# Kernel tuning notes

Hardware: AMD Instinct MI355X
Metric: run time of the kernel (lower is better)

Reference implementation:

```python
import jax, jax.numpy as jnp
import numpy as np

T, B, I, H = 1024, 64, 3, 2048


def setup_inputs() -> dict:
    key = jax.random.key(0)
    ks = jax.random.split(key, 6)
    lim = 1.0 / np.sqrt(H).astype(np.float32)  # eqx GRUCell init range
    return {
        "inp": jax.random.normal(ks[0], (T, B, I), jnp.float32),
        "init_hidden": jax.random.normal(ks[1], (B, H), jnp.float32),
        "weight_ih": jax.random.uniform(ks[2], (3 * H, I), jnp.float32, -lim, lim),
        "weight_hh": jax.random.uniform(ks[3], (3 * H, H), jnp.float32, -lim, lim),
        "bias": jax.random.uniform(ks[4], (3 * H,), jnp.float32, -lim, lim),
        "bias_n": jax.random.uniform(ks[5], (H,), jnp.float32, -lim, lim),
    }


def reference(inp, init_hidden, weight_ih, weight_hh, bias, bias_n):
    # Input projections for all timesteps at once: [T, B, 3H]
    igates_all = jnp.einsum("tbi,gi->tbg", inp, weight_ih) + bias

    def step(h, ig):
        hg = h @ weight_hh.T  # [B, 3H]
        ig_r, ig_z, ig_n = jnp.split(ig, 3, axis=-1)
        hg_r, hg_z, hg_n = jnp.split(hg, 3, axis=-1)
        reset = jax.nn.sigmoid(ig_r + hg_r)
        upd = jax.nn.sigmoid(ig_z + hg_z)
        new = jnp.tanh(ig_n + reset * (hg_n + bias_n))
        h_new = new + upd * (h - new)  # eqx GRUCell: new + inp_gate*(hidden-new)
        return h_new, h_new[:, 0]      # out = first hidden unit per step

    _, out = jax.lax.scan(step, init_hidden, igates_all)
    return out  # [T, B]
```

## Files before the change

kernel.cpp:

```cpp
#include <hip/hip_runtime.h>

typedef __attribute__((ext_vector_type(8))) short bf16x8;
typedef __attribute__((ext_vector_type(4))) float f32x4;
typedef __attribute__((ext_vector_type(4))) int i32x4;

#define Tn 1024
#define Bn 64
#define Hn 2048
#define NBLK 256
#define NTHR 512

#define GRP(ring, leaf, g) (((((ring) << 7) | ((leaf) << 3) | (g))) * 32)

#define SPIN_LIMIT (1u << 25)

__device__ __forceinline__ unsigned short f2b(float x) {
    unsigned u = __float_as_uint(x);
    return (unsigned short)((u + 0x7fffu + ((u >> 16) & 1u)) >> 16);
}
__device__ __forceinline__ float sigm(float x) {
    return __builtin_amdgcn_rcpf(1.0f + __expf(-x));
}
__device__ __forceinline__ float tanh_f(float x) {
    float e = __expf(2.0f * x);
    return 1.0f - 2.0f * __builtin_amdgcn_rcpf(1.0f + e);
}

__device__ __forceinline__ void store_short_wt(unsigned short* p, unsigned v) {
    asm volatile("global_store_short %0, %1, off sc0 sc1" :: "v"(p), "v"(v) : "memory");
}
__device__ __forceinline__ void store_dword_wt(float* p, float v) {
    asm volatile("global_store_dword %0, %1, off sc0 sc1" :: "v"(p), "v"(__float_as_uint(v)) : "memory");
}
__device__ __forceinline__ void store_u64_wt(unsigned long long* p, unsigned long long v) {
    asm volatile("global_store_dwordx2 %0, %1, off sc0 sc1" :: "v"(p), "v"(v) : "memory");
}
__device__ __forceinline__ unsigned poll_read(unsigned* p) {
    unsigned old;
    asm volatile("global_atomic_add %0, %1, %2, off sc0 sc1\n\ts_waitcnt vmcnt(0)"
                 : "=v"(old) : "v"(p), "v"(0u) : "memory");
    return old;
}

__device__ __forceinline__ long hfrag_off(int b, int k) {
    return ((long)(((k >> 5) * 4 + (b >> 4)) * 64) + ((k >> 3) & 3) * 16 + (b & 15)) * 8 + (k & 7);
}

__global__ void prep_kernel(const float* __restrict__ init_h,
                            unsigned short* __restrict__ h0,
                            unsigned* __restrict__ ctrl) {
    const int i = blockIdx.x * 256 + threadIdx.x;
    const int b  = i >> 9;
    const int k4 = (i & 511) << 2;
    float4 v = *reinterpret_cast<const float4*>(init_h + (long)b * Hn + k4);
    unsigned long long q = (unsigned long long)f2b(v.x)
                         | ((unsigned long long)f2b(v.y) << 16)
                         | ((unsigned long long)f2b(v.z) << 32)
                         | ((unsigned long long)f2b(v.w) << 48);
    store_u64_wt((unsigned long long*)(h0 + hfrag_off(b, k4)), q);
    if (i < 8192)
        asm volatile("global_store_dword %0, %1, off sc0 sc1"
                     :: "v"(ctrl + i), "v"(0u) : "memory");
}

__global__ void __launch_bounds__(NTHR, 2) gru_kernel(
    const float* __restrict__ inp,
    const float* __restrict__ init_h,
    const float* __restrict__ w_ih,
    const float* __restrict__ w_hh,
    const float* __restrict__ bias,
    const float* __restrict__ bias_n,
    unsigned short* __restrict__ h0,
    unsigned short* __restrict__ h1,
    unsigned* __restrict__ ctrl,
    float* __restrict__ out)
{
    __shared__ f32x4 red[8][2][3][64];

    const int tid  = threadIdx.x;
    const int lane = tid & 63;
    const int w    = tid >> 6;
    const int quad = lane >> 4;
    const int n16  = lane & 15;
    const int R    = blockIdx.x & 1;
    const int c    = blockIdx.x >> 1;
    const int jg   = c * 16 + n16;
    const int ks   = w * 256;
    const int bbase = 32 * R;

    bf16x8 Bf[3][8];
    #pragma unroll
    for (int nt = 0; nt < 3; ++nt) {
        const long row = (long)(nt * Hn + jg);
        #pragma unroll
        for (int k = 0; k < 8; ++k) {
            const float* p = w_hh + row * Hn + ks + k * 32 + quad * 8;
            bf16x8 b;
            #pragma unroll
            for (int j = 0; j < 8; ++j) b[j] = (short)f2b(p[j]);
            Bf[nt][k] = b;
        }
    }

    float wr0 = w_ih[jg*3+0], wr1 = w_ih[jg*3+1], wr2 = w_ih[jg*3+2];
    float wz0 = w_ih[(Hn+jg)*3+0], wz1 = w_ih[(Hn+jg)*3+1], wz2 = w_ih[(Hn+jg)*3+2];
    float wn0 = w_ih[(2*Hn+jg)*3+0], wn1 = w_ih[(2*Hn+jg)*3+1], wn2 = w_ih[(2*Hn+jg)*3+2];
    float br_ = bias[jg], bz_ = bias[Hn+jg], bn2_ = bias[2*Hn+jg];
    float bnn_ = bias_n[jg];

    float hst[4];
    if (w < 2) {
        #pragma unroll
        for (int r = 0; r < 4; ++r)
            hst[r] = init_h[(long)(bbase + 16 * w + quad * 4 + r) * Hn + jg];
    }

    const int kkE = c >> 1;
    const int qE  = (c & 1) * 2 + (n16 >> 3);
    const int eE  = n16 & 7;

    const int leafC = c >> 3;
    const int grp   = c >> 4;

    for (int t = 0; t < Tn; ++t) {
        const unsigned short* hcur = (t & 1) ? h1 : h0;
        unsigned short* hnext      = (t & 1) ? h0 : h1;

        float xv[4][3];
        if (w < 2) {
            #pragma unroll
            for (int r = 0; r < 4; ++r) {
                const float* xp = inp + ((long)t * Bn + bbase + 16 * w + quad * 4 + r) * 3;
                xv[r][0] = xp[0]; xv[r][1] = xp[1]; xv[r][2] = xp[2];
            }
        }

        f32x4 acc[2][3];
        #pragma unroll
        for (int m = 0; m < 2; ++m)
            #pragma unroll
            for (int nt = 0; nt < 3; ++nt)
                acc[m][nt] = f32x4{0.f, 0.f, 0.f, 0.f};

        if (lane == 0 && t) {
            const unsigned tgt = (unsigned)(t << 4);
            unsigned spins = 0;
            while (poll_read(&ctrl[GRP(R, leafC, w)]) < tgt) {
                __builtin_amdgcn_s_sleep(1);
                if (++spins > SPIN_LIMIT) break;
            }
        }

        const unsigned short* pa = hcur + ((long)(32 * w + 2 * R) * 64 + lane) * 8;

        i32x4 hb[16];
        #pragma unroll
        for (int kki = 0; kki < 8; ++kki) {
            #pragma unroll
            for (int m = 0; m < 2; ++m) {
                asm volatile("global_load_dwordx4 %0, %1, off sc0 sc1"
                             : "=v"(hb[kki * 2 + m])
                             : "v"(pa + (long)(kki * 4 + m) * 512) : "memory");
            }
        }
        asm volatile("s_waitcnt vmcnt(12)"
                     : "+v"(hb[0]), "+v"(hb[1]), "+v"(hb[2]), "+v"(hb[3])
                     :: "memory");
        __builtin_amdgcn_s_setprio(1);
        #pragma unroll
        for (int kki = 0; kki < 2; ++kki) {
            #pragma unroll
            for (int m = 0; m < 2; ++m) {
                union { i32x4 q; bf16x8 v; } u;
                u.q = hb[kki * 2 + m];
                bf16x8 a = u.v;
                acc[m][0] = __builtin_amdgcn_mfma_f32_16x16x32_bf16(a, Bf[0][kki], acc[m][0], 0, 0, 0);
                acc[m][1] = __builtin_amdgcn_mfma_f32_16x16x32_bf16(a, Bf[1][kki], acc[m][1], 0, 0, 0);
                acc[m][2] = __builtin_amdgcn_mfma_f32_16x16x32_bf16(a, Bf[2][kki], acc[m][2], 0, 0, 0);
            }
        }
        __builtin_amdgcn_s_setprio(0);
        asm volatile("s_waitcnt vmcnt(8)"
                     : "+v"(hb[4]), "+v"(hb[5]), "+v"(hb[6]), "+v"(hb[7])
                     :: "memory");
        __builtin_amdgcn_s_setprio(1);
        #pragma unroll
        for (int kki = 2; kki < 4; ++kki) {
            #pragma unroll
            for (int m = 0; m < 2; ++m) {
                union { i32x4 q; bf16x8 v; } u;
                u.q = hb[kki * 2 + m];
                bf16x8 a = u.v;
                acc[m][0] = __builtin_amdgcn_mfma_f32_16x16x32_bf16(a, Bf[0][kki], acc[m][0], 0, 0, 0);
                acc[m][1] = __builtin_amdgcn_mfma_f32_16x16x32_bf16(a, Bf[1][kki], acc[m][1], 0, 0, 0);
                acc[m][2] = __builtin_amdgcn_mfma_f32_16x16x32_bf16(a, Bf[2][kki], acc[m][2], 0, 0, 0);
            }
        }
        __builtin_amdgcn_s_setprio(0);
        asm volatile("s_waitcnt vmcnt(4)"
                     : "+v"(hb[8]), "+v"(hb[9]), "+v"(hb[10]), "+v"(hb[11])
                     :: "memory");
        __builtin_amdgcn_s_setprio(1);
        #pragma unroll
        for (int kki = 4; kki < 6; ++kki) {
            #pragma unroll
            for (int m = 0; m < 2; ++m) {
                union { i32x4 q; bf16x8 v; } u;
                u.q = hb[kki * 2 + m];
                bf16x8 a = u.v;
                acc[m][0] = __builtin_amdgcn_mfma_f32_16x16x32_bf16(a, Bf[0][kki], acc[m][0], 0, 0, 0);
                acc[m][1] = __builtin_amdgcn_mfma_f32_16x16x32_bf16(a, Bf[1][kki], acc[m][1], 0, 0, 0);
                acc[m][2] = __builtin_amdgcn_mfma_f32_16x16x32_bf16(a, Bf[2][kki], acc[m][2], 0, 0, 0);
            }
        }
        __builtin_amdgcn_s_setprio(0);
        asm volatile("s_waitcnt vmcnt(0)"
                     : "+v"(hb[12]), "+v"(hb[13]), "+v"(hb[14]), "+v"(hb[15])
                     :: "memory");
        __builtin_amdgcn_s_setprio(1);
        #pragma unroll
        for (int kki = 6; kki < 8; ++kki) {
            #pragma unroll
            for (int m = 0; m < 2; ++m) {
                union { i32x4 q; bf16x8 v; } u;
                u.q = hb[kki * 2 + m];
                bf16x8 a = u.v;
                acc[m][0] = __builtin_amdgcn_mfma_f32_16x16x32_bf16(a, Bf[0][kki], acc[m][0], 0, 0, 0);
                acc[m][1] = __builtin_amdgcn_mfma_f32_16x16x32_bf16(a, Bf[1][kki], acc[m][1], 0, 0, 0);
                acc[m][2] = __builtin_amdgcn_mfma_f32_16x16x32_bf16(a, Bf[2][kki], acc[m][2], 0, 0, 0);
            }
        }
        __builtin_amdgcn_s_setprio(0);

        #pragma unroll
        for (int m = 0; m < 2; ++m)
            #pragma unroll
            for (int nt = 0; nt < 3; ++nt)
                red[w][m][nt][lane] = acc[m][nt];
        __syncthreads();

        if (w < 2) {
            f32x4 s0 = red[0][w][0][lane], s1 = red[0][w][1][lane], s2 = red[0][w][2][lane];
            #pragma unroll
            for (int src = 1; src < 8; ++src) {
                s0 += red[src][w][0][lane];
                s1 += red[src][w][1][lane];
                s2 += red[src][w][2][lane];
            }
            #pragma unroll
            for (int r = 0; r < 4; ++r) {
                const int b = bbase + 16 * w + quad * 4 + r;
                float pr = br_ + wr0*xv[r][0] + wr1*xv[r][1] + wr2*xv[r][2] + s0[r];
                float pz = bz_ + wz0*xv[r][0] + wz1*xv[r][1] + wz2*xv[r][2] + s1[r];
                float rr = sigm(pr);
                float zz = sigm(pz);
                float pn = bn2_ + wn0*xv[r][0] + wn1*xv[r][1] + wn2*xv[r][2] + rr * (s2[r] + bnn_);
                float nn = tanh_f(pn);
                float hv = nn + zz * (hst[r] - nn);
                hst[r] = hv;
                store_short_wt(hnext + ((long)((kkE * 4 + 2 * R + w) * 64) + qE * 16 + quad * 4 + r) * 8 + eE,
                               (unsigned)f2b(hv));
                if (c == 0 && n16 == 0)
                    store_dword_wt(out + t * Bn + b, hv);
            }
        }

        asm volatile("s_waitcnt vmcnt(0)" ::: "memory");
        __syncthreads();
        if (tid < 16)
            __hip_atomic_fetch_add(&ctrl[GRP(R, tid, grp)], 1u,
                                   __ATOMIC_RELAXED, __HIP_MEMORY_SCOPE_SYSTEM);
    }
}

extern "C" void kernel_launch(void* const* d_in, const int* in_sizes, int n_in,
                              void* d_out, int out_size, void* d_ws, size_t ws_size,
                              hipStream_t stream) {
    const float* inp    = (const float*)d_in[0];
    const float* init_h = (const float*)d_in[1];
    const float* w_ih   = (const float*)d_in[2];
    const float* w_hh   = (const float*)d_in[3];
    const float* bias   = (const float*)d_in[4];
    const float* bias_n = (const float*)d_in[5];
    float* out = (float*)d_out;

    unsigned short* h0 = (unsigned short*)d_ws;
    unsigned short* h1 = h0 + 131072L;
    unsigned* ctrl     = (unsigned*)(h1 + 131072L);

    prep_kernel<<<128, 256, 0, stream>>>(init_h, h0, ctrl);
    gru_kernel<<<NBLK, NTHR, 0, stream>>>(inp, init_h, w_ih, w_hh, bias, bias_n,
                                          h0, h1, ctrl, out);
}
```

Before: 3.836 ms.

## Spread gate epilogue over all warps, pipeline flag polls, signal via last-arriving warp

The gate epilogue now runs on all 8 warps, one hidden element per lane, where before only 2 warps each handled 4 rows. This shortens the serial tail of each timestep. The spin-wait keeps two atomic polls in flight so each check does not pay a full round-trip latency. Cross-block signalling now comes from the last warp to finish, found through an LDS counter, rather than after the trailing __syncthreads. This lets the global flag increment go out earlier, at the cost of extra LDS atomics and more poll traffic on the control words.

```diff
diff --git a/kernel.cpp b/kernel.cpp
--- a/kernel.cpp
+++ b/kernel.cpp
@@ -34,12 +34,6 @@
 }
 __device__ __forceinline__ void store_u64_wt(unsigned long long* p, unsigned long long v) {
     asm volatile("global_store_dwordx2 %0, %1, off sc0 sc1" :: "v"(p), "v"(v) : "memory");
-}
-__device__ __forceinline__ unsigned poll_read(unsigned* p) {
-    unsigned old;
-    asm volatile("global_atomic_add %0, %1, %2, off sc0 sc1\n\ts_waitcnt vmcnt(0)"
-                 : "=v"(old) : "v"(p), "v"(0u) : "memory");
-    return old;
 }
 
 __device__ __forceinline__ long hfrag_off(int b, int k) {
@@ -76,6 +70,7 @@
     float* __restrict__ out)
 {
     __shared__ f32x4 red[8][2][3][64];
+    __shared__ unsigned lcnt;
 
     const int tid  = threadIdx.x;
     const int lane = tid & 63;
@@ -84,14 +79,13 @@
     const int n16  = lane & 15;
     const int R    = blockIdx.x & 1;
     const int c    = blockIdx.x >> 1;
-    const int jg   = c * 16 + n16;
     const int ks   = w * 256;
     const int bbase = 32 * R;
 
     bf16x8 Bf[3][8];
     #pragma unroll
     for (int nt = 0; nt < 3; ++nt) {
-        const long row = (long)(nt * Hn + jg);
+        const long row = (long)(nt * Hn + c * 16 + n16);
         #pragma unroll
         for (int k = 0; k < 8; ++k) {
             const float* p = w_hh + row * Hn + ks + k * 32 + quad * 8;
@@ -102,37 +96,39 @@
         }
     }
 
-    float wr0 = w_ih[jg*3+0], wr1 = w_ih[jg*3+1], wr2 = w_ih[jg*3+2];
-    float wz0 = w_ih[(Hn+jg)*3+0], wz1 = w_ih[(Hn+jg)*3+1], wz2 = w_ih[(Hn+jg)*3+2];
-    float wn0 = w_ih[(2*Hn+jg)*3+0], wn1 = w_ih[(2*Hn+jg)*3+1], wn2 = w_ih[(2*Hn+jg)*3+2];
-    float br_ = bias[jg], bz_ = bias[Hn+jg], bn2_ = bias[2*Hn+jg];
-    float bnn_ = bias_n[jg];
-
-    float hst[4];
-    if (w < 2) {
-        #pragma unroll
-        for (int r = 0; r < 4; ++r)
-            hst[r] = init_h[(long)(bbase + 16 * w + quad * 4 + r) * Hn + jg];
-    }
+    const int erow = 4 * w + quad;
+    const int ecol = n16;
+    const int mE   = w >> 2;
+    const int rE   = quad;
+    const int jgE  = c * 16 + ecol;
+    const int eoff = ((w & 3) * 16 + ecol) * 4 + rE;
+
+    float wr0 = w_ih[jgE*3+0], wr1 = w_ih[jgE*3+1], wr2 = w_ih[jgE*3+2];
+    float wz0 = w_ih[(Hn+jgE)*3+0], wz1 = w_ih[(Hn+jgE)*3+1], wz2 = w_ih[(Hn+jgE)*3+2];
+    float wn0 = w_ih[(2*Hn+jgE)*3+0], wn1 = w_ih[(2*Hn+jgE)*3+1], wn2 = w_ih[(2*Hn+jgE)*3+2];
+    float br_ = bias[jgE], bz_ = bias[Hn+jgE], bn2_ = bias[2*Hn+jgE];
+    float bnn_ = bias_n[jgE];
+
+    float hst = init_h[(long)(bbase + erow) * Hn + jgE];
 
     const int kkE = c >> 1;
-    const int qE  = (c & 1) * 2 + (n16 >> 3);
-    const int eE  = n16 & 7;
+    const int qE  = (c & 1) * 2 + (ecol >> 3);
+    const int eEc = ecol & 7;
 
     const int leafC = c >> 3;
     const int grp   = c >> 4;
+
+    if (tid == 0) lcnt = 0u;
+    __syncthreads();
 
     for (int t = 0; t < Tn; ++t) {
         const unsigned short* hcur = (t & 1) ? h1 : h0;
         unsigned short* hnext      = (t & 1) ? h0 : h1;
 
-        float xv[4][3];
-        if (w < 2) {
-            #pragma unroll
-            for (int r = 0; r < 4; ++r) {
-                const float* xp = inp + ((long)t * Bn + bbase + 16 * w + quad * 4 + r) * 3;
-                xv[r][0] = xp[0]; xv[r][1] = xp[1]; xv[r][2] = xp[2];
-            }
+        float xv0, xv1, xv2;
+        {
+            const float* xp = inp + ((long)t * Bn + bbase + erow) * 3;
+            xv0 = xp[0]; xv1 = xp[1]; xv2 = xp[2];
         }
 
         f32x4 acc[2][3];
@@ -144,10 +140,25 @@
 
         if (lane == 0 && t) {
             const unsigned tgt = (unsigned)(t << 4);
-            unsigned spins = 0;
-            while (poll_read(&ctrl[GRP(R, leafC, w)]) < tgt) {
+            unsigned* p = &ctrl[GRP(R, leafC, w)];
+            unsigned va, vb, spins = 0;
+            asm volatile("global_atomic_add %0, %1, %2, off sc0 sc1"
+                         : "=v"(va) : "v"(p), "v"(0u) : "memory");
+            asm volatile("global_atomic_add %0, %1, %2, off sc0 sc1"
+                         : "=v"(vb) : "v"(p), "v"(0u) : "memory");
+            for (;;) {
+                asm volatile("s_waitcnt vmcnt(1)" : "+v"(va) :: "memory");
+                if (va >= tgt) break;
                 __builtin_amdgcn_s_sleep(1);
                 if (++spins > SPIN_LIMIT) break;
+                asm volatile("global_atomic_add %0, %1, %2, off sc0 sc1"
+                             : "=v"(va) : "v"(p), "v"(0u) : "memory");
+                asm volatile("s_waitcnt vmcnt(1)" : "+v"(vb) :: "memory");
+                if (vb >= tgt) break;
+                __builtin_amdgcn_s_sleep(1);
+                if (++spins > SPIN_LIMIT) break;
+                asm volatile("global_atomic_add %0, %1, %2, off sc0 sc1"
+                             : "=v"(vb) : "v"(p), "v"(0u) : "memory");
             }
         }
 
@@ -239,37 +250,39 @@
                 red[w][m][nt][lane] = acc[m][nt];
         __syncthreads();
 
-        if (w < 2) {
-            f32x4 s0 = red[0][w][0][lane], s1 = red[0][w][1][lane], s2 = red[0][w][2][lane];
-            #pragma unroll
-            for (int src = 1; src < 8; ++src) {
-                s0 += red[src][w][0][lane];
-                s1 += red[src][w][1][lane];
-                s2 += red[src][w][2][lane];
-            }
-            #pragma unroll
-            for (int r = 0; r < 4; ++r) {
-                const int b = bbase + 16 * w + quad * 4 + r;
-                float pr = br_ + wr0*xv[r][0] + wr1*xv[r][1] + wr2*xv[r][2] + s0[r];
-                float pz = bz_ + wz0*xv[r][0] + wz1*xv[r][1] + wz2*xv[r][2] + s1[r];
-                float rr = sigm(pr);
-                float zz = sigm(pz);
-                float pn = bn2_ + wn0*xv[r][0] + wn1*xv[r][1] + wn2*xv[r][2] + rr * (s2[r] + bnn_);
-                float nn = tanh_f(pn);
-                float hv = nn + zz * (hst[r] - nn);
-                hst[r] = hv;
-                store_short_wt(hnext + ((long)((kkE * 4 + 2 * R + w) * 64) + qE * 16 + quad * 4 + r) * 8 + eE,
-                               (unsigned)f2b(hv));
-                if (c == 0 && n16 == 0)
-                    store_dword_wt(out + t * Bn + b, hv);
-            }
+        {
+            const float* redf = (const float*)red;
+            float s0 = 0.f, s1 = 0.f, s2 = 0.f;
+            #pragma unroll
+            for (int src = 0; src < 8; ++src) {
+                const int pb = (src * 2 + mE) * 3;
+                s0 += redf[(pb + 0) * 256 + eoff];
+                s1 += redf[(pb + 1) * 256 + eoff];
+                s2 += redf[(pb + 2) * 256 + eoff];
+            }
+            float pr = br_ + wr0*xv0 + wr1*xv1 + wr2*xv2 + s0;
+            float pz = bz_ + wz0*xv0 + wz1*xv1 + wz2*xv2 + s1;
+            float rr = sigm(pr);
+            float zz = sigm(pz);
+            float pn = bn2_ + wn0*xv0 + wn1*xv1 + wn2*xv2 + rr * (s2 + bnn_);
+            float nn = tanh_f(pn);
+            float hv = nn + zz * (hst - nn);
+            hst = hv;
+            store_short_wt(hnext + ((long)((kkE * 4 + 2 * R + mE) * 64)
+                                    + qE * 16 + 4 * (w & 3) + rE) * 8 + eEc,
+                           (unsigned)f2b(hv));
+            if (c == 0 && ecol == 0)
+                store_dword_wt(out + t * Bn + bbase + erow, hv);
         }
 
         asm volatile("s_waitcnt vmcnt(0)" ::: "memory");
+        unsigned old = 0;
+        if (lane == 0) old = atomicAdd(&lcnt, 1u);
+        old = __shfl(old, 0);
+        if (((old & 7u) == 7u) && lane < 16)
+            __hip_atomic_fetch_add(&ctrl[GRP(R, lane, grp)], 1u,
+                                   __ATOMIC_RELAXED, __HIP_MEMORY_SCOPE_SYSTEM);
         __syncthreads();
-        if (tid < 16)
-            __hip_atomic_fetch_add(&ctrl[GRP(R, tid, grp)], 1u,
-                                   __ATOMIC_RELAXED, __HIP_MEMORY_SCOPE_SYSTEM);
     }
 }
 
```

New measurement: 3.943 ms. +2.8%, slower.

## Pipeline barrier polling with two in-flight atomics and last-wave signaling

Applied to the files above, without the earlier changes.

The spin-wait now keeps two atomic poll reads in flight at once and alternates between them, so each check waits on an older request rather than a full round trip. The cross-block arrival signal is no longer sent after __syncthreads; an LDS counter picks out the last of the 8 waves to finish its stores, and that wave issues the 16 global increments. This moves the signal ahead of the block barrier and is meant to cut inter-block latency in the per-timestep grid sync. The risks are extra atomic traffic from the doubled polling, and relying on vmcnt(0) in every wave to order the stores before the signal.

```diff
diff --git a/kernel.cpp b/kernel.cpp
--- a/kernel.cpp
+++ b/kernel.cpp
@@ -34,12 +34,6 @@
 }
 __device__ __forceinline__ void store_u64_wt(unsigned long long* p, unsigned long long v) {
     asm volatile("global_store_dwordx2 %0, %1, off sc0 sc1" :: "v"(p), "v"(v) : "memory");
-}
-__device__ __forceinline__ unsigned poll_read(unsigned* p) {
-    unsigned old;
-    asm volatile("global_atomic_add %0, %1, %2, off sc0 sc1\n\ts_waitcnt vmcnt(0)"
-                 : "=v"(old) : "v"(p), "v"(0u) : "memory");
-    return old;
 }
 
 __device__ __forceinline__ long hfrag_off(int b, int k) {
@@ -76,6 +70,7 @@
     float* __restrict__ out)
 {
     __shared__ f32x4 red[8][2][3][64];
+    __shared__ unsigned lcnt;
 
     const int tid  = threadIdx.x;
     const int lane = tid & 63;
@@ -122,6 +117,9 @@
     const int leafC = c >> 3;
     const int grp   = c >> 4;
 
+    if (tid == 0) lcnt = 0u;
+    __syncthreads();
+
     for (int t = 0; t < Tn; ++t) {
         const unsigned short* hcur = (t & 1) ? h1 : h0;
         unsigned short* hnext      = (t & 1) ? h0 : h1;
@@ -144,10 +142,25 @@
 
         if (lane == 0 && t) {
             const unsigned tgt = (unsigned)(t << 4);
-            unsigned spins = 0;
-            while (poll_read(&ctrl[GRP(R, leafC, w)]) < tgt) {
+            unsigned* p = &ctrl[GRP(R, leafC, w)];
+            unsigned va, vb, spins = 0;
+            asm volatile("global_atomic_add %0, %1, %2, off sc0 sc1"
+                         : "=v"(va) : "v"(p), "v"(0u) : "memory");
+            asm volatile("global_atomic_add %0, %1, %2, off sc0 sc1"
+                         : "=v"(vb) : "v"(p), "v"(0u) : "memory");
+            for (;;) {
+                asm volatile("s_waitcnt vmcnt(1)" : "+v"(va) :: "memory");
+                if (va >= tgt) break;
                 __builtin_amdgcn_s_sleep(1);
                 if (++spins > SPIN_LIMIT) break;
+                asm volatile("global_atomic_add %0, %1, %2, off sc0 sc1"
+                             : "=v"(va) : "v"(p), "v"(0u) : "memory");
+                asm volatile("s_waitcnt vmcnt(1)" : "+v"(vb) :: "memory");
+                if (vb >= tgt) break;
+                __builtin_amdgcn_s_sleep(1);
+                if (++spins > SPIN_LIMIT) break;
+                asm volatile("global_atomic_add %0, %1, %2, off sc0 sc1"
+                             : "=v"(vb) : "v"(p), "v"(0u) : "memory");
             }
         }
 
@@ -266,10 +279,13 @@
         }
 
         asm volatile("s_waitcnt vmcnt(0)" ::: "memory");
+        unsigned old = 0;
+        if (lane == 0) old = atomicAdd(&lcnt, 1u);
+        old = __shfl(old, 0);
+        if (((old & 7u) == 7u) && lane < 16)
+            __hip_atomic_fetch_add(&ctrl[GRP(R, lane, grp)], 1u,
+                                   __ATOMIC_RELAXED, __HIP_MEMORY_SCOPE_SYSTEM);
         __syncthreads();
-        if (tid < 16)
-            __hip_atomic_fetch_add(&ctrl[GRP(R, tid, grp)], 1u,
-                                   __ATOMIC_RELAXED, __HIP_MEMORY_SCOPE_SYSTEM);
     }
 }
 
```

New measurement: 3.962 ms. +3.3%, slower.
